# Kernel optimization log

Hardware: AMD Instinct MI355X
Metric: run time of the kernel (lower is better)

## Reference

```python
import jax, jax.numpy as jnp
import numpy as np

N_NODES = 50000
N_EDGES = 800000
IN_FEATS = 256
N_HEADS = 4
OUT_FEATS = 32
NEG_SLOPE = 0.2


def setup_inputs() -> dict:
    key = jax.random.key(0)
    k_feat, k_src, k_dst, k_fc, k_al, k_ar, k_res = jax.random.split(key, 7)
    feat = jax.random.normal(k_feat, (N_NODES, IN_FEATS), dtype=jnp.float32)
    src = jax.random.randint(k_src, (N_EDGES,), 0, N_NODES)
    dst = jax.random.randint(k_dst, (N_EDGES,), 0, N_NODES)
    # xavier-normal-ish scales
    s_fc = (2.0 / (IN_FEATS + N_HEADS * OUT_FEATS)) ** 0.5
    W_fc = jax.random.normal(k_fc, (N_HEADS * OUT_FEATS, IN_FEATS), dtype=jnp.float32) * s_fc
    s_a = (2.0 / (1 + N_HEADS * OUT_FEATS)) ** 0.5
    attn_l = jax.random.normal(k_al, (N_HEADS, OUT_FEATS), dtype=jnp.float32) * s_a
    attn_r = jax.random.normal(k_ar, (N_HEADS, OUT_FEATS), dtype=jnp.float32) * s_a
    W_res = jax.random.normal(k_res, (N_HEADS * OUT_FEATS, IN_FEATS), dtype=jnp.float32) * s_fc
    return {"feat": feat, "src": src, "dst": dst, "W_fc": W_fc,
            "attn_l": attn_l, "attn_r": attn_r, "W_res": W_res}


def reference(feat, src, dst, W_fc, attn_l, attn_r, W_res):
    N = feat.shape[0]
    H, D = attn_l.shape
    ones_e = jnp.ones(src.shape[0], dtype=feat.dtype)

    # projection: [N, H, D]
    h = (feat @ W_fc.T).reshape(N, H, D)
    feat_dst = h  # dst features are pre-norm (torch code aliases before * norm)

    # symmetric norm on source side: out_degree^-0.5
    out_deg = jax.ops.segment_sum(ones_e, src, num_segments=N)
    feat_src = h * (jnp.clip(out_deg, 1.0) ** -0.5)[:, None, None]

    # per-node attention halves -> per-edge score, leaky relu
    el = jnp.einsum('nhd,hd->nh', feat_src, attn_l)  # [N, H]
    er = jnp.einsum('nhd,hd->nh', feat_dst, attn_r)  # [N, H]
    e = jax.nn.leaky_relu(el[src] + er[dst], NEG_SLOPE)  # [E, H]

    # edge_softmax over incoming edges of each dst node
    emax = jax.ops.segment_max(e, dst, num_segments=N)
    emax = jnp.where(jnp.isfinite(emax), emax, 0.0)  # guard empty segments
    ex = jnp.exp(e - emax[dst])
    denom = jax.ops.segment_sum(ex, dst, num_segments=N)
    a = ex / denom[dst]  # [E, H]

    # weighted scatter-sum of messages: u_mul_e + sum
    msg = feat_src[src] * a[:, :, None]  # [E, H, D]
    rst = jax.ops.segment_sum(msg, dst, num_segments=N)  # [N, H, D]

    # symmetric norm on destination side: in_degree^0.5
    in_deg = jax.ops.segment_sum(ones_e, dst, num_segments=N)
    rst = rst * jnp.sqrt(jnp.clip(in_deg, 1.0))[:, None, None]

    # residual projection
    rst = rst + (feat @ W_res.T).reshape(N, H, D)
    return rst
```

## Files before the change

### kernel.cpp

```cpp
#include <hip/hip_runtime.h>
#include <hip/hip_bf16.h>
#include <math.h>

#define HD 128
#define IN_F 256
#define NEG_SLOPE 0.2f
#define NMAX 50000
#define GGRID 256

typedef __attribute__((ext_vector_type(8))) short short8;
typedef __attribute__((ext_vector_type(4))) float f32x4;

__device__ __forceinline__ unsigned short f2bf(float x) {
    __hip_bfloat16 b = __float2bfloat16(x);
    return *(unsigned short*)&b;
}
__device__ __forceinline__ float bf2f(unsigned short u) {
    unsigned int v = ((unsigned int)u) << 16;
    float f;
    __builtin_memcpy(&f, &v, 4);
    return f;
}
__device__ __forceinline__ short8 pack8(float4 f0, float4 f1) {
    short8 v;
    v[0] = (short)f2bf(f0.x); v[1] = (short)f2bf(f0.y);
    v[2] = (short)f2bf(f0.z); v[3] = (short)f2bf(f0.w);
    v[4] = (short)f2bf(f1.x); v[5] = (short)f2bf(f1.y);
    v[6] = (short)f2bf(f1.z); v[7] = (short)f2bf(f1.w);
    return v;
}

__global__ void cvt_w_kernel(const float4* __restrict__ wfc, const float4* __restrict__ wres,
                             ushort4* __restrict__ w16, int n4each) {
    int idx = blockIdx.x * blockDim.x + threadIdx.x;
    if (idx >= 2 * n4each) return;
    float4 f = (idx < n4each) ? wfc[idx] : wres[idx - n4each];
    ushort4 u;
    u.x = f2bf(f.x); u.y = f2bf(f.y); u.z = f2bf(f.z); u.w = f2bf(f.w);
    w16[idx] = u;
}

__global__ __launch_bounds__(256) void ew_kernel(const float* __restrict__ wfc,
                                                 const float* __restrict__ attn_l,
                                                 const float* __restrict__ attn_r,
                                                 unsigned short* __restrict__ ew16) {
    int h = blockIdx.x;
    int k = threadIdx.x;
    float sl = 0.f, sr = 0.f;
#pragma unroll 8
    for (int d = 0; d < 32; d++) {
        float w = wfc[(size_t)(h * 32 + d) * IN_F + k];
        sl += attn_l[h * 32 + d] * w;
        sr += attn_r[h * 32 + d] * w;
    }
    ew16[h * IN_F + k] = f2bf(sl);
    ew16[(4 + h) * IN_F + k] = f2bf(sr);
    ew16[(8 + h) * IN_F + k] = 0;
    ew16[(12 + h) * IN_F + k] = 0;
}

__global__ __launch_bounds__(512) void hist_kernel(const int* __restrict__ src,
                                                   const int* __restrict__ dst,
                                                   unsigned short* __restrict__ pc_src,
                                                   unsigned short* __restrict__ pc_dst,
                                                   int N, int E, int chunk) {
    __shared__ unsigned int h[NMAX / 2];
    int tid = threadIdx.x;
    int nh = N >> 1;
    uint4* h4 = (uint4*)h;
    for (int i = tid; i < (nh >> 2); i += 512) h4[i] = make_uint4(0, 0, 0, 0);
    for (int i = (nh & ~3) + tid; i < nh; i += 512) h[i] = 0;
    __syncthreads();

    const int* arr = blockIdx.y ? src : dst;
    int e1 = min(E, (int)(blockIdx.x + 1) * chunk);
    for (int e = blockIdx.x * chunk + tid; e < e1; e += 512) {
        int v = arr[e];
        atomicAdd(&h[v >> 1], 1u << ((v & 1) << 4));
    }
    __syncthreads();

    unsigned short* pc = (blockIdx.y ? pc_src : pc_dst) + (size_t)blockIdx.x * N;
    uint4* pc4 = (uint4*)pc;
    for (int i = tid; i < (nh >> 2); i += 512) pc4[i] = h4[i];
    for (int i = (nh & ~3) + tid; i < nh; i += 512) ((unsigned int*)pc)[i] = h[i];
}

__global__ __launch_bounds__(256) void sum_scan1_kernel(
    const unsigned short* __restrict__ pc_src, unsigned short* __restrict__ pc_dst,
    int* __restrict__ out_cnt, int* __restrict__ deg, int* __restrict__ bsum,
    int N, int C) {
    __shared__ int wsum[4];
    int n = blockIdx.x * 256 + threadIdx.x;
    int sd = 0;
    if (n < N) {
        int ss = 0;
        for (int c = 0; c < C; c++) {
            ss += pc_src[(size_t)c * N + n];
            unsigned short v = pc_dst[(size_t)c * N + n];
            pc_dst[(size_t)c * N + n] = (unsigned short)sd;
            sd += v;
        }
        out_cnt[n] = ss;
        deg[n] = sd;
    }
    int v = (n < N) ? sd : 0;
#pragma unroll
    for (int d = 1; d < 64; d <<= 1) v += __shfl_xor(v, d);
    if ((threadIdx.x & 63) == 0) wsum[threadIdx.x >> 6] = v;
    __syncthreads();
    if (threadIdx.x == 0) bsum[blockIdx.x] = wsum[0] + wsum[1] + wsum[2] + wsum[3];
}

__global__ __launch_bounds__(256) void scan2_kernel(int* __restrict__ bsum, int nb,
                                                    int* __restrict__ row_start_N, int E) {
    __shared__ int wtot[4];
    int tid = threadIdx.x, lane = tid & 63, wid = tid >> 6;
    int v = (tid < nb) ? bsum[tid] : 0;
    int incl = v;
#pragma unroll
    for (int d = 1; d < 64; d <<= 1) {
        int t = __shfl_up(incl, d);
        if (lane >= d) incl += t;
    }
    if (lane == 63) wtot[wid] = incl;
    __syncthreads();
    int woff = 0;
    for (int w = 0; w < wid; w++) woff += wtot[w];
    if (tid < nb) bsum[tid] = woff + incl - v;
    if (tid == 0) *row_start_N = E;
}

__global__ __launch_bounds__(256) void scan3_kernel(const int* __restrict__ deg,
                                                    const int* __restrict__ boff,
                                                    int* __restrict__ row_start, int N) {
    __shared__ int wsum[4];
    int i = blockIdx.x * 256 + threadIdx.x;
    int lane = threadIdx.x & 63, wid = threadIdx.x >> 6;
    int v = (i < N) ? deg[i] : 0;
    int incl = v;
#pragma unroll
    for (int d = 1; d < 64; d <<= 1) {
        int t = __shfl_up(incl, d);
        if (lane >= d) incl += t;
    }
    if (lane == 63) wsum[wid] = incl;
    __syncthreads();
    int woff = 0;
    for (int w = 0; w < wid; w++) woff += wsum[w];
    int excl = boff[blockIdx.x] + woff + incl - v;
    if (i < N) row_start[i] = excl;
}

__global__ __launch_bounds__(512) void place_kernel(const int* __restrict__ src,
                                                    const int* __restrict__ dst,
                                                    const unsigned short* __restrict__ chunkpre,
                                                    const int* __restrict__ row_start,
                                                    int* __restrict__ esrc,
                                                    int N, int E, int chunk) {
    __shared__ unsigned int cur[NMAX / 2];
    int tid = threadIdx.x;
    int nh = N >> 1;
    const unsigned short* cp = chunkpre + (size_t)blockIdx.x * N;
    const uint4* cp4 = (const uint4*)cp;
    uint4* cur4 = (uint4*)cur;
    for (int i = tid; i < (nh >> 2); i += 512) cur4[i] = cp4[i];
    for (int i = (nh & ~3) + tid; i < nh; i += 512) cur[i] = ((const unsigned int*)cp)[i];
    __syncthreads();

    int e1 = min(E, (int)(blockIdx.x + 1) * chunk);
    for (int e = blockIdx.x * chunk + tid; e < e1; e += 512) {
        int d = dst[e], s = src[e];
        int sh = (d & 1) << 4;
        unsigned int old = atomicAdd(&cur[d >> 1], 1u << sh);
        int rank = (old >> sh) & 0xffff;
        esrc[row_start[d] + rank] = s;
    }
}

__global__ __launch_bounds__(512, 1) void gemm_fused(
    const float* __restrict__ feat, const __hip_bfloat16* __restrict__ w16,
    const __hip_bfloat16* __restrict__ ew16, const int* __restrict__ out_cnt,
    unsigned short* __restrict__ h16, unsigned short* __restrict__ resid16,
    float* __restrict__ el, float* __restrict__ er, int N, int ntiles) {
    __shared__ unsigned short sB[256 * 256];
    __shared__ unsigned short sA[32 * 256];
    int tid = threadIdx.x;
    int lane = tid & 63, w = tid >> 6;
    int l15 = lane & 15, lg = lane >> 4;
    int c0 = w * 32;
    bool w0 = (w == 0);
    bool isH = (w < 4);
    int colloc = c0 & 127;

#pragma unroll
    for (int it = 0; it < 16; ++it) {
        int idx = it * 512 + tid;
        int c = idx >> 5, g = idx & 31;
        short8 v = *(const short8*)(w16 + (size_t)c * IN_F + g * 8);
        *(short8*)&sB[c * 256 + ((g ^ (c & 7)) * 8)] = v;
    }
    short8 ereg[8];
    if (w0) {
        const __hip_bfloat16* ep = ew16 + (size_t)l15 * IN_F + lg * 8;
#pragma unroll
        for (int kk = 0; kk < 8; kk++) ereg[kk] = *(const short8*)(ep + kk * 32);
    }

    int srow[2], sgc[2];
#pragma unroll
    for (int i = 0; i < 2; i++) {
        int idx = i * 512 + tid;
        srow[i] = idx >> 5;
        sgc[i] = idx & 31;
    }

    float4 fA[2][2];
    int t = blockIdx.x;
#pragma unroll
    for (int i = 0; i < 2; i++) {
        int gm = t * 32 + srow[i];
        gm = (gm < N) ? gm : (N - 1);
        const float4* fp = (const float4*)(feat + (size_t)gm * IN_F + sgc[i] * 8);
        fA[i][0] = fp[0];
        fA[i][1] = fp[1];
    }

    for (; t < ntiles; t += GGRID) {
        __syncthreads();
#pragma unroll
        for (int i = 0; i < 2; i++)
            *(short8*)&sA[srow[i] * 256 + ((sgc[i] ^ (srow[i] & 7)) * 8)] =
                pack8(fA[i][0], fA[i][1]);
        __syncthreads();

        int tn = t + GGRID;
        if (tn < ntiles) {
#pragma unroll
            for (int i = 0; i < 2; i++) {
                int gm = tn * 32 + srow[i];
                gm = (gm < N) ? gm : (N - 1);
                const float4* fp = (const float4*)(feat + (size_t)gm * IN_F + sgc[i] * 8);
                fA[i][0] = fp[0];
                fA[i][1] = fp[1];
            }
        }

        f32x4 acc[2][2], accE[2];
#pragma unroll
        for (int i = 0; i < 2; i++) {
            accE[i] = (f32x4){0.f, 0.f, 0.f, 0.f};
#pragma unroll
            for (int j = 0; j < 2; j++) acc[i][j] = (f32x4){0.f, 0.f, 0.f, 0.f};
        }
#pragma unroll
        for (int kk = 0; kk < 8; kk++) {
            short8 a[2], b[2];
#pragma unroll
            for (int mi = 0; mi < 2; mi++) {
                int row = mi * 16 + l15;
                int gs = (kk * 4 + lg) ^ (row & 7);
                a[mi] = *(const short8*)&sA[row * 256 + gs * 8];
            }
#pragma unroll
            for (int ni = 0; ni < 2; ni++) {
                int c = c0 + ni * 16 + l15;
                int gsb = (kk * 4 + lg) ^ (c & 7);
                b[ni] = *(const short8*)&sB[c * 256 + gsb * 8];
            }
#pragma unroll
            for (int mi = 0; mi < 2; mi++)
#pragma unroll
                for (int ni = 0; ni < 2; ni++)
                    acc[mi][ni] = __builtin_amdgcn_mfma_f32_16x16x32_bf16(
                        a[mi], b[ni], acc[mi][ni], 0, 0, 0);
            if (w0) {
#pragma unroll
                for (int mi = 0; mi < 2; mi++)
                    accE[mi] = __builtin_amdgcn_mfma_f32_16x16x32_bf16(
                        a[mi], ereg[kk], accE[mi], 0, 0, 0);
            }
        }

        int bm = t * 32;
#pragma unroll
        for (int mi = 0; mi < 2; mi++) {
#pragma unroll
            for (int reg = 0; reg < 4; reg++) {
                int r = bm + mi * 16 + lg * 4 + reg;
                bool valid = (r < N);
                int rr = valid ? r : 0;
                if (isH) {
                    float nrm = rsqrtf(fmaxf((float)out_cnt[rr], 1.0f));
                    if (valid) {
#pragma unroll
                        for (int ni = 0; ni < 2; ni++)
                            h16[(size_t)r * HD + colloc + ni * 16 + l15] =
                                f2bf(acc[mi][ni][reg] * nrm);
                        if (w0) {
                            float ev = accE[mi][reg];
                            if (l15 < 4) el[r * 4 + l15] = ev * nrm;
                            else if (l15 < 8) er[r * 4 + (l15 - 4)] = ev;
                        }
                    }
                } else if (valid) {
#pragma unroll
                    for (int ni = 0; ni < 2; ni++)
                        resid16[(size_t)r * HD + colloc + ni * 16 + l15] =
                            f2bf(acc[mi][ni][reg]);
                }
            }
        }
    }
}

__global__ __launch_bounds__(256) void agg_kernel(const unsigned short* __restrict__ h16,
                                                  const float* __restrict__ el,
                                                  const float* __restrict__ er,
                                                  const int* __restrict__ row_start,
                                                  const int* __restrict__ esrc,
                                                  const unsigned short* __restrict__ resid16,
                                                  float* __restrict__ out, int N) {
    int wid = threadIdx.x >> 6, lane = threadIdx.x & 63;
    int n = blockIdx.x * 4 + wid;
    if (n >= N) return;
    int es = lane >> 4;
    int l15 = lane & 15;
    int h = l15 >> 2;
    int d0 = l15 * 8;
    int beg = row_start[n], end = row_start[n + 1];
    float erh = er[n * 4 + h];
    float den = 0.f;
    float acc[8];
#pragma unroll
    for (int j = 0; j < 8; j++) acc[j] = 0.f;

    if (beg < end) {
        bool ok0, ok1;
        float ev0, ev1; short8 hv0, hv1;
        {
            int i0 = beg + es, i1 = beg + 4 + es;
            ok0 = i0 < end; ok1 = i1 < end;
            int s0 = esrc[ok0 ? i0 : beg];
            int s1 = esrc[ok1 ? i1 : beg];
            ev0 = el[s0 * 4 + h]; ev1 = el[s1 * 4 + h];
            hv0 = *(const short8*)(h16 + (size_t)s0 * HD + d0);
            hv1 = *(const short8*)(h16 + (size_t)s1 * HD + d0);
        }
        for (int base = beg + 8; base < end; base += 8) {
            int i0 = base + es, i1 = base + 4 + es;
            bool p0 = i0 < end, p1 = i1 < end;
            int t0 = esrc[p0 ? i0 : beg];
            int t1 = esrc[p1 ? i1 : beg];
            float fv0 = el[t0 * 4 + h];
            float fv1 = el[t1 * 4 + h];
            short8 g0 = *(const short8*)(h16 + (size_t)t0 * HD + d0);
            short8 g1 = *(const short8*)(h16 + (size_t)t1 * HD + d0);
            float e0 = ev0 + erh; e0 = (e0 > 0.f) ? e0 : NEG_SLOPE * e0;
            float e1 = ev1 + erh; e1 = (e1 > 0.f) ? e1 : NEG_SLOPE * e1;
            float ex0 = ok0 ? __expf(e0) : 0.f;
            float ex1 = ok1 ? __expf(e1) : 0.f;
            den += ex0 + ex1;
#pragma unroll
            for (int j = 0; j < 8; j++)
                acc[j] += ex0 * bf2f((unsigned short)hv0[j]) +
                          ex1 * bf2f((unsigned short)hv1[j]);
            ok0 = p0; ok1 = p1; ev0 = fv0; ev1 = fv1; hv0 = g0; hv1 = g1;
        }
        float e0 = ev0 + erh; e0 = (e0 > 0.f) ? e0 : NEG_SLOPE * e0;
        float e1 = ev1 + erh; e1 = (e1 > 0.f) ? e1 : NEG_SLOPE * e1;
        float ex0 = ok0 ? __expf(e0) : 0.f;
        float ex1 = ok1 ? __expf(e1) : 0.f;
        den += ex0 + ex1;
#pragma unroll
        for (int j = 0; j < 8; j++)
            acc[j] += ex0 * bf2f((unsigned short)hv0[j]) +
                      ex1 * bf2f((unsigned short)hv1[j]);
    }

#pragma unroll
    for (int m = 16; m < 64; m <<= 1) {
        den += __shfl_xor(den, m);
#pragma unroll
        for (int j = 0; j < 8; j++) acc[j] += __shfl_xor(acc[j], m);
    }

    if (es == 0) {
        const unsigned short* rp = resid16 + (size_t)n * HD + d0;
        short8 rv = *(const short8*)rp;
        int indeg = end - beg;
        float sc = (indeg > 0) ? sqrtf((float)indeg) / den : 0.f;
        float o[8];
#pragma unroll
        for (int j = 0; j < 8; j++)
            o[j] = sc * acc[j] + bf2f((unsigned short)rv[j]);
        float* op = out + (size_t)n * HD + d0;
        *(float4*)op = make_float4(o[0], o[1], o[2], o[3]);
        *(float4*)(op + 4) = make_float4(o[4], o[5], o[6], o[7]);
    }
}

extern "C" void kernel_launch(void* const* d_in, const int* in_sizes, int n_in,
                              void* d_out, int out_size, void* d_ws, size_t ws_size,
                              hipStream_t stream) {
    const float* feat   = (const float*)d_in[0];
    const int*   src    = (const int*)d_in[1];
    const int*   dst    = (const int*)d_in[2];
    const float* W_fc   = (const float*)d_in[3];
    const float* attn_l = (const float*)d_in[4];
    const float* attn_r = (const float*)d_in[5];
    const float* W_res  = (const float*)d_in[6];
    float* out = (float*)d_out;

    int N = in_sizes[0] / IN_F;
    int E = in_sizes[1];
    int nb = (N + 255) / 256;

    size_t off = 0;
    auto alloc = [&](size_t bytes) {
        size_t o = off;
        off = (off + bytes + 255) & ~(size_t)255;
        return o;
    };
    char* ws = (char*)d_ws;
    unsigned short* h16     = (unsigned short*)(ws + alloc((size_t)N * HD * 2));
    unsigned short* resid16 = (unsigned short*)(ws + alloc((size_t)N * HD * 2));
    __hip_bfloat16* w16     = (__hip_bfloat16*)(ws + alloc((size_t)2 * HD * IN_F * 2));
    unsigned short* ew16    = (unsigned short*)(ws + alloc((size_t)16 * IN_F * 2));
    float* el               = (float*)(ws + alloc((size_t)N * 4 * 4));
    float* er               = (float*)(ws + alloc((size_t)N * 4 * 4));
    int* out_cnt            = (int*)(ws + alloc((size_t)N * 4));
    int* deg                = (int*)(ws + alloc((size_t)N * 4));
    int* row_start          = (int*)(ws + alloc((size_t)(N + 1) * 4));
    int* bsum               = (int*)(ws + alloc((size_t)nb * 4));
    int* esrc               = (int*)(ws + alloc((size_t)E * 4));

    size_t per_chunk = (size_t)4 * N;
    size_t avail = (ws_size > off + 4096) ? (ws_size - off - 4096) : 0;
    int C = (int)(avail / per_chunk);
    if (C > 128) C = 128;
    if (C < 32) C = 32;
    unsigned short* pc_dst = (unsigned short*)(ws + alloc((size_t)C * N * 2));
    unsigned short* pc_src = (unsigned short*)(ws + alloc((size_t)C * N * 2));
    int chunk = (E + C - 1) / C;

    int n4each = HD * IN_F / 4;
    cvt_w_kernel<<<(2 * n4each + 255) / 256, 256, 0, stream>>>(
        (const float4*)W_fc, (const float4*)W_res, (ushort4*)w16, n4each);
    ew_kernel<<<4, 256, 0, stream>>>(W_fc, attn_l, attn_r, ew16);

    hist_kernel<<<dim3(C, 2), 512, 0, stream>>>(src, dst, pc_src, pc_dst, N, E, chunk);
    sum_scan1_kernel<<<nb, 256, 0, stream>>>(pc_src, pc_dst, out_cnt, deg, bsum, N, C);
    scan2_kernel<<<1, 256, 0, stream>>>(bsum, nb, row_start + N, E);
    scan3_kernel<<<nb, 256, 0, stream>>>(deg, bsum, row_start, N);
    place_kernel<<<C, 512, 0, stream>>>(src, dst, pc_dst, row_start, esrc, N, E, chunk);

    int ntiles = (N + 31) / 32;
    gemm_fused<<<GGRID, 512, 0, stream>>>(feat, (const __hip_bfloat16*)w16,
                                          (const __hip_bfloat16*)ew16, out_cnt,
                                          h16, resid16, el, er, N, ntiles);

    int nb4 = (N + 3) / 4;
    agg_kernel<<<nb4, 256, 0, stream>>>(h16, el, er, row_start, esrc, resid16, out, N);
}
```

Before: 144.5 us.

## Merge small kernels, shrink source histogram chunks, deepen agg edge prefetch

Merges the weight conversion and attention-weight kernels into one launch. Folds the block-offset scan into scan3 by having every block rescan the block sums. Gives the source-degree histogram a fixed 32 chunks instead of C, which shrinks the partial-count buffer and the reduction loop. The aggregation kernel now processes 16 edges per iteration with a 4-deep register prefetch instead of 8. Together these cut launch count and memory traffic, at the cost of more registers in the aggregation kernel and redundant scan work per block.

```diff
diff --git a/kernel.cpp b/kernel.cpp
--- a/kernel.cpp
+++ b/kernel.cpp
@@ -7,6 +7,7 @@
 #define NEG_SLOPE 0.2f
 #define NMAX 50000
 #define GGRID 256
+#define CSRC 32
 
 typedef __attribute__((ext_vector_type(8))) short short8;
 typedef __attribute__((ext_vector_type(4))) float f32x4;
@@ -30,40 +31,41 @@
     return v;
 }
 
-__global__ void cvt_w_kernel(const float4* __restrict__ wfc, const float4* __restrict__ wres,
-                             ushort4* __restrict__ w16, int n4each) {
-    int idx = blockIdx.x * blockDim.x + threadIdx.x;
+__global__ __launch_bounds__(256) void cvt_ew_kernel(
+    const float4* __restrict__ wfc4, const float4* __restrict__ wres4,
+    const float* __restrict__ wfc, const float* __restrict__ attn_l,
+    const float* __restrict__ attn_r, ushort4* __restrict__ w16,
+    unsigned short* __restrict__ ew16, int n4each) {
+    int b = blockIdx.x;
+    if (b < 4) {
+        int h = b, k = threadIdx.x;
+        float sl = 0.f, sr = 0.f;
+#pragma unroll 8
+        for (int d = 0; d < 32; d++) {
+            float w = wfc[(size_t)(h * 32 + d) * IN_F + k];
+            sl += attn_l[h * 32 + d] * w;
+            sr += attn_r[h * 32 + d] * w;
+        }
+        ew16[h * IN_F + k] = f2bf(sl);
+        ew16[(4 + h) * IN_F + k] = f2bf(sr);
+        ew16[(8 + h) * IN_F + k] = 0;
+        ew16[(12 + h) * IN_F + k] = 0;
+        return;
+    }
+    int idx = (b - 4) * 256 + threadIdx.x;
     if (idx >= 2 * n4each) return;
-    float4 f = (idx < n4each) ? wfc[idx] : wres[idx - n4each];
+    float4 f = (idx < n4each) ? wfc4[idx] : wres4[idx - n4each];
     ushort4 u;
     u.x = f2bf(f.x); u.y = f2bf(f.y); u.z = f2bf(f.z); u.w = f2bf(f.w);
     w16[idx] = u;
-}
-
-__global__ __launch_bounds__(256) void ew_kernel(const float* __restrict__ wfc,
-                                                 const float* __restrict__ attn_l,
-                                                 const float* __restrict__ attn_r,
-                                                 unsigned short* __restrict__ ew16) {
-    int h = blockIdx.x;
-    int k = threadIdx.x;
-    float sl = 0.f, sr = 0.f;
-#pragma unroll 8
-    for (int d = 0; d < 32; d++) {
-        float w = wfc[(size_t)(h * 32 + d) * IN_F + k];
-        sl += attn_l[h * 32 + d] * w;
-        sr += attn_r[h * 32 + d] * w;
-    }
-    ew16[h * IN_F + k] = f2bf(sl);
-    ew16[(4 + h) * IN_F + k] = f2bf(sr);
-    ew16[(8 + h) * IN_F + k] = 0;
-    ew16[(12 + h) * IN_F + k] = 0;
 }
 
 __global__ __launch_bounds__(512) void hist_kernel(const int* __restrict__ src,
                                                    const int* __restrict__ dst,
                                                    unsigned short* __restrict__ pc_src,
                                                    unsigned short* __restrict__ pc_dst,
-                                                   int N, int E, int chunk) {
+                                                   int N, int E, int C, int chunk,
+                                                   int chunk_s) {
     __shared__ unsigned int h[NMAX / 2];
     int tid = threadIdx.x;
     int nh = N >> 1;
@@ -72,15 +74,19 @@
     for (int i = (nh & ~3) + tid; i < nh; i += 512) h[i] = 0;
     __syncthreads();
 
-    const int* arr = blockIdx.y ? src : dst;
-    int e1 = min(E, (int)(blockIdx.x + 1) * chunk);
-    for (int e = blockIdx.x * chunk + tid; e < e1; e += 512) {
+    int b = blockIdx.x;
+    bool isSrc = (b >= C);
+    const int* arr = isSrc ? src : dst;
+    int c = isSrc ? (b - C) : b;
+    int ch = isSrc ? chunk_s : chunk;
+    int e0 = c * ch, e1 = min(E, (c + 1) * ch);
+    for (int e = e0 + tid; e < e1; e += 512) {
         int v = arr[e];
         atomicAdd(&h[v >> 1], 1u << ((v & 1) << 4));
     }
     __syncthreads();
 
-    unsigned short* pc = (blockIdx.y ? pc_src : pc_dst) + (size_t)blockIdx.x * N;
+    unsigned short* pc = (isSrc ? pc_src : pc_dst) + (size_t)c * N;
     uint4* pc4 = (uint4*)pc;
     for (int i = tid; i < (nh >> 2); i += 512) pc4[i] = h4[i];
     for (int i = (nh & ~3) + tid; i < nh; i += 512) ((unsigned int*)pc)[i] = h[i];
@@ -95,8 +101,9 @@
     int sd = 0;
     if (n < N) {
         int ss = 0;
+#pragma unroll 4
+        for (int c = 0; c < CSRC; c++) ss += pc_src[(size_t)c * N + n];
         for (int c = 0; c < C; c++) {
-            ss += pc_src[(size_t)c * N + n];
             unsigned short v = pc_dst[(size_t)c * N + n];
             pc_dst[(size_t)c * N + n] = (unsigned short)sd;
             sd += v;
@@ -112,43 +119,45 @@
     if (threadIdx.x == 0) bsum[blockIdx.x] = wsum[0] + wsum[1] + wsum[2] + wsum[3];
 }
 
-__global__ __launch_bounds__(256) void scan2_kernel(int* __restrict__ bsum, int nb,
-                                                    int* __restrict__ row_start_N, int E) {
-    __shared__ int wtot[4];
+__global__ __launch_bounds__(256) void scan3_kernel(const int* __restrict__ deg,
+                                                    const int* __restrict__ bsum,
+                                                    int* __restrict__ row_start,
+                                                    int N, int nb, int E) {
+    __shared__ int wsum[4];
+    __shared__ int sbo[256];
     int tid = threadIdx.x, lane = tid & 63, wid = tid >> 6;
-    int v = (tid < nb) ? bsum[tid] : 0;
+    {
+        int v = (tid < nb) ? bsum[tid] : 0;
+        int incl = v;
+#pragma unroll
+        for (int d = 1; d < 64; d <<= 1) {
+            int t = __shfl_up(incl, d);
+            if (lane >= d) incl += t;
+        }
+        if (lane == 63) wsum[wid] = incl;
+        __syncthreads();
+        int woff = 0;
+        for (int w = 0; w < wid; w++) woff += wsum[w];
+        sbo[tid] = woff + incl - v;
+        __syncthreads();
+    }
+    int boff = sbo[blockIdx.x];
+    if (blockIdx.x == 0 && tid == 0) row_start[N] = E;
+    __syncthreads();
+
+    int i = blockIdx.x * 256 + tid;
+    int v = (i < N) ? deg[i] : 0;
     int incl = v;
 #pragma unroll
     for (int d = 1; d < 64; d <<= 1) {
         int t = __shfl_up(incl, d);
         if (lane >= d) incl += t;
     }
-    if (lane == 63) wtot[wid] = incl;
-    __syncthreads();
-    int woff = 0;
-    for (int w = 0; w < wid; w++) woff += wtot[w];
-    if (tid < nb) bsum[tid] = woff + incl - v;
-    if (tid == 0) *row_start_N = E;
-}
-
-__global__ __launch_bounds__(256) void scan3_kernel(const int* __restrict__ deg,
-                                                    const int* __restrict__ boff,
-                                                    int* __restrict__ row_start, int N) {
-    __shared__ int wsum[4];
-    int i = blockIdx.x * 256 + threadIdx.x;
-    int lane = threadIdx.x & 63, wid = threadIdx.x >> 6;
-    int v = (i < N) ? deg[i] : 0;
-    int incl = v;
-#pragma unroll
-    for (int d = 1; d < 64; d <<= 1) {
-        int t = __shfl_up(incl, d);
-        if (lane >= d) incl += t;
-    }
     if (lane == 63) wsum[wid] = incl;
     __syncthreads();
     int woff = 0;
     for (int w = 0; w < wid; w++) woff += wsum[w];
-    int excl = boff[blockIdx.x] + woff + incl - v;
+    int excl = boff + woff + incl - v;
     if (i < N) row_start[i] = excl;
 }
 
@@ -336,46 +345,38 @@
     for (int j = 0; j < 8; j++) acc[j] = 0.f;
 
     if (beg < end) {
-        bool ok0, ok1;
-        float ev0, ev1; short8 hv0, hv1;
-        {
-            int i0 = beg + es, i1 = beg + 4 + es;
-            ok0 = i0 < end; ok1 = i1 < end;
-            int s0 = esrc[ok0 ? i0 : beg];
-            int s1 = esrc[ok1 ? i1 : beg];
-            ev0 = el[s0 * 4 + h]; ev1 = el[s1 * 4 + h];
-            hv0 = *(const short8*)(h16 + (size_t)s0 * HD + d0);
-            hv1 = *(const short8*)(h16 + (size_t)s1 * HD + d0);
-        }
-        for (int base = beg + 8; base < end; base += 8) {
-            int i0 = base + es, i1 = base + 4 + es;
-            bool p0 = i0 < end, p1 = i1 < end;
-            int t0 = esrc[p0 ? i0 : beg];
-            int t1 = esrc[p1 ? i1 : beg];
-            float fv0 = el[t0 * 4 + h];
-            float fv1 = el[t1 * 4 + h];
-            short8 g0 = *(const short8*)(h16 + (size_t)t0 * HD + d0);
-            short8 g1 = *(const short8*)(h16 + (size_t)t1 * HD + d0);
-            float e0 = ev0 + erh; e0 = (e0 > 0.f) ? e0 : NEG_SLOPE * e0;
-            float e1 = ev1 + erh; e1 = (e1 > 0.f) ? e1 : NEG_SLOPE * e1;
-            float ex0 = ok0 ? __expf(e0) : 0.f;
-            float ex1 = ok1 ? __expf(e1) : 0.f;
-            den += ex0 + ex1;
-#pragma unroll
-            for (int j = 0; j < 8; j++)
-                acc[j] += ex0 * bf2f((unsigned short)hv0[j]) +
-                          ex1 * bf2f((unsigned short)hv1[j]);
-            ok0 = p0; ok1 = p1; ev0 = fv0; ev1 = fv1; hv0 = g0; hv1 = g1;
-        }
-        float e0 = ev0 + erh; e0 = (e0 > 0.f) ? e0 : NEG_SLOPE * e0;
-        float e1 = ev1 + erh; e1 = (e1 > 0.f) ? e1 : NEG_SLOPE * e1;
-        float ex0 = ok0 ? __expf(e0) : 0.f;
-        float ex1 = ok1 ? __expf(e1) : 0.f;
-        den += ex0 + ex1;
-#pragma unroll
-        for (int j = 0; j < 8; j++)
-            acc[j] += ex0 * bf2f((unsigned short)hv0[j]) +
-                      ex1 * bf2f((unsigned short)hv1[j]);
+        bool ok[4]; float ev[4]; short8 hv[4];
+        auto LOAD = [&](int base, bool* okk, float* evv, short8* hvv) {
+#pragma unroll
+            for (int u = 0; u < 4; u++) {
+                int idx = base + u * 4 + es;
+                okk[u] = idx < end;
+                int s = esrc[okk[u] ? idx : beg];
+                evv[u] = el[s * 4 + h];
+                hvv[u] = *(const short8*)(h16 + (size_t)s * HD + d0);
+            }
+        };
+        auto COMPUTE = [&](const bool* okk, const float* evv, const short8* hvv) {
+#pragma unroll
+            for (int u = 0; u < 4; u++) {
+                float e = evv[u] + erh;
+                e = (e > 0.f) ? e : NEG_SLOPE * e;
+                float ex = okk[u] ? __expf(e) : 0.f;
+                den += ex;
+#pragma unroll
+                for (int j = 0; j < 8; j++)
+                    acc[j] += ex * bf2f((unsigned short)hvv[u][j]);
+            }
+        };
+        LOAD(beg, ok, ev, hv);
+        for (int base = beg + 16; base < end; base += 16) {
+            bool ok2[4]; float ev2[4]; short8 hv2[4];
+            LOAD(base, ok2, ev2, hv2);
+            COMPUTE(ok, ev, hv);
+#pragma unroll
+            for (int u = 0; u < 4; u++) { ok[u] = ok2[u]; ev[u] = ev2[u]; hv[u] = hv2[u]; }
+        }
+        COMPUTE(ok, ev, hv);
     }
 
 #pragma unroll
@@ -434,25 +435,27 @@
     int* row_start          = (int*)(ws + alloc((size_t)(N + 1) * 4));
     int* bsum               = (int*)(ws + alloc((size_t)nb * 4));
     int* esrc               = (int*)(ws + alloc((size_t)E * 4));
-
-    size_t per_chunk = (size_t)4 * N;
+    unsigned short* pc_src  = (unsigned short*)(ws + alloc((size_t)CSRC * N * 2));
+
+    size_t per_chunk = (size_t)2 * N;
     size_t avail = (ws_size > off + 4096) ? (ws_size - off - 4096) : 0;
     int C = (int)(avail / per_chunk);
     if (C > 128) C = 128;
     if (C < 32) C = 32;
     unsigned short* pc_dst = (unsigned short*)(ws + alloc((size_t)C * N * 2));
-    unsigned short* pc_src = (unsigned short*)(ws + alloc((size_t)C * N * 2));
     int chunk = (E + C - 1) / C;
+    int chunk_s = (E + CSRC - 1) / CSRC;
 
     int n4each = HD * IN_F / 4;
-    cvt_w_kernel<<<(2 * n4each + 255) / 256, 256, 0, stream>>>(
-        (const float4*)W_fc, (const float4*)W_res, (ushort4*)w16, n4each);
-    ew_kernel<<<4, 256, 0, stream>>>(W_fc, attn_l, attn_r, ew16);
-
-    hist_kernel<<<dim3(C, 2), 512, 0, stream>>>(src, dst, pc_src, pc_dst, N, E, chunk);
+    int cvtb = (2 * n4each + 255) / 256;
+    cvt_ew_kernel<<<4 + cvtb, 256, 0, stream>>>(
+        (const float4*)W_fc, (const float4*)W_res, W_fc, attn_l, attn_r,
+        (ushort4*)w16, ew16, n4each);
+
+    hist_kernel<<<C + CSRC, 512, 0, stream>>>(src, dst, pc_src, pc_dst,
+                                              N, E, C, chunk, chunk_s);
     sum_scan1_kernel<<<nb, 256, 0, stream>>>(pc_src, pc_dst, out_cnt, deg, bsum, N, C);
-    scan2_kernel<<<1, 256, 0, stream>>>(bsum, nb, row_start + N, E);
-    scan3_kernel<<<nb, 256, 0, stream>>>(deg, bsum, row_start, N);
+    scan3_kernel<<<nb, 256, 0, stream>>>(deg, bsum, row_start, N, nb, E);
     place_kernel<<<C, 512, 0, stream>>>(src, dst, pc_dst, row_start, esrc, N, E, chunk);
 
     int ntiles = (N + 31) / 32;
```

Measured after the change: 148.7 us. 2.9% more time.
